# Performance work log

Hardware: AMD Instinct MI355X
Metric: run time of the kernel (lower is better)

The kernel has to match this reference:

```python
import jax, jax.numpy as jnp
import numpy as np

N, E, D, ED, G = 100000, 1600000, 64, 64, 512  # nodes, edges, node_dim, edge_dim, graphs
LN_EPS = 1e-5


def setup_inputs() -> dict:
    key = jax.random.key(0)
    ks = jax.random.split(key, 16)
    s_e = 1.0 / np.sqrt(ED)
    s_n = 1.0 / np.sqrt(D)
    inp = {
        'x': jax.random.normal(ks[0], (N, D), jnp.float32),
        'edge_index': jax.random.randint(ks[1], (2, E), 0, N, dtype=jnp.int32),
        'edge_attr': jax.random.normal(ks[2], (E, ED), jnp.float32),
        'node2graph': jnp.sort(jax.random.randint(ks[3], (N,), 0, G, dtype=jnp.int32)),
        # conv1 params
        'We1': jax.random.normal(ks[4], (ED, D), jnp.float32) * s_e,
        'be1': jnp.zeros((D,), jnp.float32),
        'Wm1': jax.random.normal(ks[5], (D, D), jnp.float32) * s_n,
        'bm1': jnp.zeros((D,), jnp.float32),
        'eps1': jnp.array([0.1], jnp.float32),
        'gamma1': jnp.ones((D,), jnp.float32),
        'beta1': jnp.zeros((D,), jnp.float32),
        # conv2 params
        'We2': jax.random.normal(ks[6], (ED, D), jnp.float32) * s_e,
        'be2': jnp.zeros((D,), jnp.float32),
        'Wm2': jax.random.normal(ks[7], (D, D), jnp.float32) * s_n,
        'bm2': jnp.zeros((D,), jnp.float32),
        'eps2': jnp.array([0.1], jnp.float32),
        'gamma2': jnp.ones((D,), jnp.float32),
        'beta2': jnp.zeros((D,), jnp.float32),
    }
    return inp


def _gine_conv(x, src, dst, edge_attr, We, be, Wm, bm, eps):
    # message: SiLU(Wm @ relu(x_j + SiLU(We @ e)) )  gathered per edge, scatter-added to dst
    ea = jax.nn.silu(edge_attr @ We + be)                     # (E, D)
    msg = jax.nn.silu(jnp.maximum(x[src] + ea, 0.0) @ Wm + bm)  # (E, D)
    agg = jax.ops.segment_sum(msg, dst, num_segments=x.shape[0])
    return agg + (1.0 + eps) * x


def _graph_norm(x, g, gamma, beta):
    # pyg LayerNorm(mode='graph'): normalize over all nodes*channels per graph
    f = x.shape[1]
    cnt = jax.ops.segment_sum(jnp.ones((x.shape[0],), x.dtype), g, num_segments=G) * f
    cnt = jnp.maximum(cnt, 1.0)
    mean = jax.ops.segment_sum(x.sum(-1), g, num_segments=G) / cnt          # (G,)
    var = jax.ops.segment_sum((x * x).sum(-1), g, num_segments=G) / cnt - mean ** 2
    xn = (x - mean[g][:, None]) / jnp.sqrt(var + LN_EPS)[g][:, None]
    return xn * gamma + beta


def reference(x, edge_index, edge_attr, node2graph,
              We1, be1, Wm1, bm1, eps1, gamma1, beta1,
              We2, be2, Wm2, bm2, eps2, gamma2, beta2):
    src, dst = edge_index[0], edge_index[1]
    identity = x
    # branch 1 (NOTE: the original torch code computes conv1->norm->relu but then
    # overwrites `out` with conv2(x, ...); we reproduce that faithfully)
    out = _gine_conv(x, src, dst, edge_attr, We1, be1, Wm1, bm1, eps1)
    out = _graph_norm(out, node2graph, gamma1, beta1)
    out = jnp.maximum(out, 0.0)
    # branch 2 (takes original x, per source)
    out = _gine_conv(x, src, dst, edge_attr, We2, be2, Wm2, bm2, eps2)
    out = _graph_norm(out, node2graph, gamma2, beta2)
    out = out + identity
    return jnp.maximum(out, 0.0)
```

## Files before the change

kernel.cpp:

```cpp
#include <hip/hip_runtime.h>
#include <math.h>

#define NN 100000
#define NE 1600000
#define NG 512
#define LN_EPS 1e-5f

typedef __attribute__((ext_vector_type(8))) short short8;
typedef __attribute__((ext_vector_type(4))) float floatx4;

union BF8 { short8 v; short s[8]; };
union F4  { floatx4 v; float f[4]; };

static __device__ __forceinline__ short f2bf(float f) {
    union { float f; unsigned u; } a; a.f = f;
    unsigned u = a.u;
    unsigned r = (u + 0x7fffu + ((u >> 16) & 1u)) >> 16;
    return (short)r;
}
static __device__ __forceinline__ float silu_f(float v) {
    return v / (1.0f + __expf(-v));
}

__global__ __launch_bounds__(256)
void hist_kernel(const int* __restrict__ dst, int* __restrict__ cnt)
{
    for (int e = blockIdx.x * blockDim.x + threadIdx.x; e < NE;
         e += gridDim.x * blockDim.x)
        atomicAdd(&cnt[dst[e]], 1);
}

#define SCAN_CHUNK 1024
#define SCAN_NB ((NN + SCAN_CHUNK - 1) / SCAN_CHUNK)

__global__ __launch_bounds__(256)
void scan_partial_kernel(const int* __restrict__ cnt, int* __restrict__ bsums)
{
    __shared__ int sdata[256];
    const int b = blockIdx.x, t = threadIdx.x;
    const int base = b * SCAN_CHUNK + t * 4;
    int s = 0;
    #pragma unroll
    for (int i = 0; i < 4; ++i) {
        const int idx = base + i;
        s += (idx < NN) ? cnt[idx] : 0;
    }
    sdata[t] = s;
    __syncthreads();
    for (int off = 128; off > 0; off >>= 1) {
        if (t < off) sdata[t] += sdata[t + off];
        __syncthreads();
    }
    if (t == 0) bsums[b] = sdata[0];
}

__global__ __launch_bounds__(128)
void scan_top_kernel(int* __restrict__ bsums)
{
    __shared__ int s[128];
    const int t = threadIdx.x;
    const int v = (t < SCAN_NB) ? bsums[t] : 0;
    s[t] = v;
    __syncthreads();
    for (int off = 1; off < 128; off <<= 1) {
        const int u = (t >= off) ? s[t - off] : 0;
        __syncthreads();
        s[t] += u;
        __syncthreads();
    }
    if (t < SCAN_NB) bsums[t] = s[t] - v;
}

__global__ __launch_bounds__(256)
void scan_final_kernel(int* __restrict__ cnt, const int* __restrict__ bsums)
{
    __shared__ int sdata[256];
    const int b = blockIdx.x, t = threadIdx.x;
    const int base = b * SCAN_CHUNK + t * 4;
    int c[4];
    #pragma unroll
    for (int i = 0; i < 4; ++i) {
        const int idx = base + i;
        c[i] = (idx < NN) ? cnt[idx] : 0;
    }
    const int tsum = c[0] + c[1] + c[2] + c[3];
    sdata[t] = tsum;
    __syncthreads();
    for (int off = 1; off < 256; off <<= 1) {
        const int v = (t >= off) ? sdata[t - off] : 0;
        __syncthreads();
        sdata[t] += v;
        __syncthreads();
    }
    int off0 = bsums[b] + sdata[t] - tsum;
    #pragma unroll
    for (int i = 0; i < 4; ++i) {
        const int idx = base + i;
        if (idx < NN) cnt[idx] = off0;
        off0 += c[i];
    }
}

__global__ __launch_bounds__(256)
void scatter_kernel(const int* __restrict__ src, const int* __restrict__ dst,
                    int* __restrict__ starts,
                    int2* __restrict__ ps, int* __restrict__ dsts_s)
{
    for (int e = blockIdx.x * blockDim.x + threadIdx.x; e < NE;
         e += gridDim.x * blockDim.x) {
        const int d = dst[e];
        const int pos = atomicAdd(&starts[d], 1);
        ps[pos] = make_int2(e, src[e]);
        dsts_s[pos] = d;
    }
}

#define EK_BLOCKS 1024
#define EK_WAVES (EK_BLOCKS * 4)

__global__ __launch_bounds__(256)
void edge_kernel_sorted(const float* __restrict__ x,
                        const int2* __restrict__ ps,
                        const int* __restrict__ dsts_s,
                        const float* __restrict__ eattr,
                        const float* __restrict__ We,
                        const float* __restrict__ be,
                        const float* __restrict__ Wm,
                        const float* __restrict__ bm,
                        float* __restrict__ agg)
{
    __shared__ float ltile[4][16 * 68];
    const int lane = threadIdx.x & 63;
    const int wid  = threadIdx.x >> 6;
    const int m = lane & 15;
    const int q = lane >> 4;
    float* tile = ltile[wid];

    short8 wef[2][4], wmf[2][4];
    float bev[4], bmv[4];
    #pragma unroll
    for (int kh = 0; kh < 2; ++kh)
        #pragma unroll
        for (int t = 0; t < 4; ++t) {
            BF8 fe, fm;
            #pragma unroll
            for (int j = 0; j < 8; ++j) {
                const int k = kh * 32 + q * 8 + j;
                const int n = m + 16 * t;
                fe.s[j] = f2bf(We[k * 64 + n]);
                fm.s[j] = f2bf(Wm[k * 64 + n]);
            }
            wef[kh][t] = fe.v; wmf[kh][t] = fm.v;
        }
    #pragma unroll
    for (int t = 0; t < 4; ++t) { bev[t] = be[m + 16 * t]; bmv[t] = bm[m + 16 * t]; }

    const int n_tiles = NE / 16;
    const int tpw = (n_tiles + EK_WAVES - 1) / EK_WAVES;
    const int w = blockIdx.x * 4 + wid;
    const int tl0 = w * tpw;
    const int tl1 = min(n_tiles, tl0 + tpw);
    if (tl0 >= tl1) return;

    int2 pv = ps[tl0 * 16 + m];
    int4 dnv = *(const int4*)&dsts_s[tl0 * 16 + q * 4];
    floatx4 ea[4];
    {
        const float* p = eattr + (size_t)pv.x * 64 + q * 8;
        ea[0] = *(const floatx4*)p;        ea[1] = *(const floatx4*)(p + 4);
        ea[2] = *(const floatx4*)(p + 32); ea[3] = *(const floatx4*)(p + 36);
    }

    float cv[4] = {0.f, 0.f, 0.f, 0.f};
    int cd = -1;

    for (int tl = tl0; tl < tl1; ++tl) {
        const bool haveNext = (tl + 1 < tl1);
        int2 pvn = pv; int4 dnn = dnv; floatx4 ean[4];
        if (haveNext) {
            const int e0n = (tl + 1) * 16;
            pvn = ps[e0n + m];
            dnn = *(const int4*)&dsts_s[e0n + q * 4];
            const float* p = eattr + (size_t)pvn.x * 64 + q * 8;
            ean[0] = *(const floatx4*)p;        ean[1] = *(const floatx4*)(p + 4);
            ean[2] = *(const floatx4*)(p + 32); ean[3] = *(const floatx4*)(p + 36);
        }
        floatx4 xv[4];
        {
            const float* xp = x + (size_t)pv.y * 64 + q * 8;
            xv[0] = *(const floatx4*)xp;        xv[1] = *(const floatx4*)(xp + 4);
            xv[2] = *(const floatx4*)(xp + 32); xv[3] = *(const floatx4*)(xp + 36);
        }

        short8 a1[2];
        {
            F4 u0, u1, u2, u3;
            u0.v = ea[0]; u1.v = ea[1]; u2.v = ea[2]; u3.v = ea[3];
            BF8 f0, f1;
            #pragma unroll
            for (int j = 0; j < 4; ++j) {
                f0.s[j] = f2bf(u0.f[j]); f0.s[j + 4] = f2bf(u1.f[j]);
                f1.s[j] = f2bf(u2.f[j]); f1.s[j + 4] = f2bf(u3.f[j]);
            }
            a1[0] = f0.v; a1[1] = f1.v;
        }
        floatx4 acc[4];
        #pragma unroll
        for (int t = 0; t < 4; ++t) acc[t] = (floatx4){0.f, 0.f, 0.f, 0.f};
        #pragma unroll
        for (int kh = 0; kh < 2; ++kh)
            #pragma unroll
            for (int t = 0; t < 4; ++t)
                acc[t] = __builtin_amdgcn_mfma_f32_16x16x32_bf16(a1[kh], wef[kh][t], acc[t], 0, 0, 0);

        #pragma unroll
        for (int t = 0; t < 4; ++t)
            #pragma unroll
            for (int r = 0; r < 4; ++r)
                tile[(q * 4 + r) * 68 + m + 16 * t] = silu_f(acc[t][r] + bev[t]);
        __asm__ volatile("s_waitcnt lgkmcnt(0)" ::: "memory");

        short8 a2[2];
        {
            const float* lp = &tile[m * 68 + q * 8];
            floatx4 t0 = *(const floatx4*)lp;        floatx4 t1 = *(const floatx4*)(lp + 4);
            floatx4 t2 = *(const floatx4*)(lp + 32); floatx4 t3 = *(const floatx4*)(lp + 36);
            F4 a, b, c, d, X0, X1, X2, X3;
            a.v = t0; b.v = t1; c.v = t2; d.v = t3;
            X0.v = xv[0]; X1.v = xv[1]; X2.v = xv[2]; X3.v = xv[3];
            BF8 f0, f1;
            #pragma unroll
            for (int j = 0; j < 4; ++j) {
                f0.s[j]     = f2bf(fmaxf(a.f[j] + X0.f[j], 0.0f));
                f0.s[j + 4] = f2bf(fmaxf(b.f[j] + X1.f[j], 0.0f));
                f1.s[j]     = f2bf(fmaxf(c.f[j] + X2.f[j], 0.0f));
                f1.s[j + 4] = f2bf(fmaxf(d.f[j] + X3.f[j], 0.0f));
            }
            a2[0] = f0.v; a2[1] = f1.v;
        }
        #pragma unroll
        for (int t = 0; t < 4; ++t) acc[t] = (floatx4){0.f, 0.f, 0.f, 0.f};
        #pragma unroll
        for (int kh = 0; kh < 2; ++kh)
            #pragma unroll
            for (int t = 0; t < 4; ++t)
                acc[t] = __builtin_amdgcn_mfma_f32_16x16x32_bf16(a2[kh], wmf[kh][t], acc[t], 0, 0, 0);

        float sv[4][4];
        #pragma unroll
        for (int t = 0; t < 4; ++t)
            #pragma unroll
            for (int r = 0; r < 4; ++r)
                sv[t][r] = silu_f(acc[t][r] + bmv[t]);

        const int dn[4] = {dnv.x, dnv.y, dnv.z, dnv.w};
        #define FLUSH(DN, VAL)                                                  \
            do {                                                                \
                atomicAdd(agg + (size_t)(DN) * 64 + m,      (VAL)[0]);          \
                atomicAdd(agg + (size_t)(DN) * 64 + m + 16, (VAL)[1]);          \
                atomicAdd(agg + (size_t)(DN) * 64 + m + 32, (VAL)[2]);          \
                atomicAdd(agg + (size_t)(DN) * 64 + m + 48, (VAL)[3]);          \
            } while (0)

        float run[4], head[4] = {0.f, 0.f, 0.f, 0.f};
        const int hd = dn[0];
        int rd = dn[0];
        bool headClosed = false;
        #pragma unroll
        for (int t = 0; t < 4; ++t) run[t] = sv[t][0];
        #pragma unroll
        for (int r = 1; r < 4; ++r) {
            if (dn[r] == rd) {
                #pragma unroll
                for (int t = 0; t < 4; ++t) run[t] += sv[t][r];
            } else {
                if (!headClosed) {
                    #pragma unroll
                    for (int t = 0; t < 4; ++t) head[t] = run[t];
                    headClosed = true;
                } else {
                    FLUSH(rd, run);
                }
                #pragma unroll
                for (int t = 0; t < 4; ++t) run[t] = sv[t][r];
                rd = dn[r];
            }
        }
        const bool pure = !headClosed;
        float tail[4]; const int td = rd;
        #pragma unroll
        for (int t = 0; t < 4; ++t) tail[t] = run[t];

        float tl_[4]; int td_;
        #pragma unroll
        for (int t = 0; t < 4; ++t) tl_[t] = tail[t];
        td_ = td;
        #pragma unroll
        for (int g = 0; g < 4; ++g) {
            float iv[4]; int ivd;
            if (g == 0) {
                #pragma unroll
                for (int t = 0; t < 4; ++t) iv[t] = cv[t];
                ivd = cd;
            } else {
                const int sl = m + (g - 1) * 16;
                #pragma unroll
                for (int t = 0; t < 4; ++t) iv[t] = __shfl(tl_[t], sl, 64);
                ivd = __shfl(td_, (g - 1) * 16, 64);
            }
            const int hdg = __shfl(hd, g * 16, 64);
            const bool mine = (q == g);
            if (ivd == hdg) {
                if (mine) {
                    if (pure) {
                        #pragma unroll
                        for (int t = 0; t < 4; ++t) tl_[t] += iv[t];
                    } else {
                        #pragma unroll
                        for (int t = 0; t < 4; ++t) head[t] += iv[t];
                    }
                }
            } else {
                if (g == 0) {
                    if (q == 0 && cd >= 0) FLUSH(cd, iv);
                } else {
                    if (q == g - 1) FLUSH(td_, tl_);
                }
            }
            if (mine && !pure) FLUSH(hd, head);
        }
        #pragma unroll
        for (int t = 0; t < 4; ++t) cv[t] = __shfl(tl_[t], m + 48, 64);
        cd = __shfl(td_, 48, 64);

        pv = pvn; dnv = dnn;
        #pragma unroll
        for (int t = 0; t < 4; ++t) ea[t] = ean[t];
    }
    if (q == 0 && cd >= 0) {
        atomicAdd(agg + (size_t)cd * 64 + m,      cv[0]);
        atomicAdd(agg + (size_t)cd * 64 + m + 16, cv[1]);
        atomicAdd(agg + (size_t)cd * 64 + m + 32, cv[2]);
        atomicAdd(agg + (size_t)cd * 64 + m + 48, cv[3]);
    }
    #undef FLUSH
}

__global__ __launch_bounds__(256)
void edge_kernel_unsorted(const float* __restrict__ x,
                          const int* __restrict__ src,
                          const int* __restrict__ dst,
                          const float* __restrict__ eattr,
                          const float* __restrict__ We,
                          const float* __restrict__ be,
                          const float* __restrict__ Wm,
                          const float* __restrict__ bm,
                          float* __restrict__ agg)
{
    __shared__ float ltile[4][16 * 68];
    const int lane = threadIdx.x & 63;
    const int wid  = threadIdx.x >> 6;
    const int m = lane & 15;
    const int q = lane >> 4;
    float* tile = ltile[wid];

    short8 wef[2][4], wmf[2][4];
    float bev[4], bmv[4];
    #pragma unroll
    for (int kh = 0; kh < 2; ++kh)
        #pragma unroll
        for (int t = 0; t < 4; ++t) {
            BF8 fe, fm;
            #pragma unroll
            for (int j = 0; j < 8; ++j) {
                const int k = kh * 32 + q * 8 + j;
                const int n = m + 16 * t;
                fe.s[j] = f2bf(We[k * 64 + n]);
                fm.s[j] = f2bf(Wm[k * 64 + n]);
            }
            wef[kh][t] = fe.v; wmf[kh][t] = fm.v;
        }
    #pragma unroll
    for (int t = 0; t < 4; ++t) { bev[t] = be[m + 16 * t]; bmv[t] = bm[m + 16 * t]; }

    const int n_tiles = NE / 16;
    const int stride = gridDim.x * 4;
    for (int tl = blockIdx.x * 4 + wid; tl < n_tiles; tl += stride) {
        const int e0 = tl * 16;
        short8 a1[2];
        #pragma unroll
        for (int kh = 0; kh < 2; ++kh) {
            const float* p = eattr + (size_t)(e0 + m) * 64 + kh * 32 + q * 8;
            F4 v0, v1; v0.v = *(const floatx4*)p; v1.v = *(const floatx4*)(p + 4);
            BF8 f;
            #pragma unroll
            for (int j = 0; j < 4; ++j) { f.s[j] = f2bf(v0.f[j]); f.s[j + 4] = f2bf(v1.f[j]); }
            a1[kh] = f.v;
        }
        floatx4 acc[4];
        #pragma unroll
        for (int t = 0; t < 4; ++t) acc[t] = (floatx4){0.f, 0.f, 0.f, 0.f};
        #pragma unroll
        for (int kh = 0; kh < 2; ++kh)
            #pragma unroll
            for (int t = 0; t < 4; ++t)
                acc[t] = __builtin_amdgcn_mfma_f32_16x16x32_bf16(a1[kh], wef[kh][t], acc[t], 0, 0, 0);
        #pragma unroll
        for (int t = 0; t < 4; ++t)
            #pragma unroll
            for (int r = 0; r < 4; ++r)
                tile[(q * 4 + r) * 68 + m + 16 * t] = silu_f(acc[t][r] + bev[t]);
        __asm__ volatile("s_waitcnt lgkmcnt(0)" ::: "memory");
        const int sn = src[e0 + m];
        short8 a2[2];
        {
            const float* lp = &tile[m * 68 + q * 8];
            const float* xp = x + (size_t)sn * 64 + q * 8;
            F4 a, b, c, d, X0, X1, X2, X3;
            a.v = *(const floatx4*)lp;        b.v = *(const floatx4*)(lp + 4);
            c.v = *(const floatx4*)(lp + 32); d.v = *(const floatx4*)(lp + 36);
            X0.v = *(const floatx4*)xp;        X1.v = *(const floatx4*)(xp + 4);
            X2.v = *(const floatx4*)(xp + 32); X3.v = *(const floatx4*)(xp + 36);
            BF8 f0, f1;
            #pragma unroll
            for (int j = 0; j < 4; ++j) {
                f0.s[j]     = f2bf(fmaxf(a.f[j] + X0.f[j], 0.0f));
                f0.s[j + 4] = f2bf(fmaxf(b.f[j] + X1.f[j], 0.0f));
                f1.s[j]     = f2bf(fmaxf(c.f[j] + X2.f[j], 0.0f));
                f1.s[j + 4] = f2bf(fmaxf(d.f[j] + X3.f[j], 0.0f));
            }
            a2[0] = f0.v; a2[1] = f1.v;
        }
        #pragma unroll
        for (int t = 0; t < 4; ++t) acc[t] = (floatx4){0.f, 0.f, 0.f, 0.f};
        #pragma unroll
        for (int kh = 0; kh < 2; ++kh)
            #pragma unroll
            for (int t = 0; t < 4; ++t)
                acc[t] = __builtin_amdgcn_mfma_f32_16x16x32_bf16(a2[kh], wmf[kh][t], acc[t], 0, 0, 0);
        int dn[4];
        #pragma unroll
        for (int r = 0; r < 4; ++r) dn[r] = dst[e0 + q * 4 + r];
        #pragma unroll
        for (int t = 0; t < 4; ++t)
            #pragma unroll
            for (int r = 0; r < 4; ++r)
                atomicAdd(agg + (size_t)dn[r] * 64 + m + 16 * t, silu_f(acc[t][r] + bmv[t]));
    }
}

#define STATS_WAVES 4096
__global__ __launch_bounds__(256)
void stats_kernel(const float* __restrict__ agg,
                  const float* __restrict__ x,
                  const int* __restrict__ n2g,
                  const float* __restrict__ eps,
                  float* __restrict__ gsum,
                  float* __restrict__ gss,
                  float* __restrict__ gcnt)
{
    const int lane = threadIdx.x & 63;
    const int wid  = threadIdx.x >> 6;
    const int w    = blockIdx.x * 4 + wid;
    const int chunk = (NN + STATS_WAVES - 1) / STATS_WAVES;
    const int n0 = w * chunk;
    const int n1 = min(NN, n0 + chunk);
    if (n0 >= n1) return;
    const float k = 1.0f + eps[0];

    int   curg = n2g[n0];
    float s = 0.f, ss = 0.f, rc = 0.f;
    for (int n = n0; n < n1; ++n) {
        const int g = n2g[n];
        if (g != curg) {
            float a = s, b = ss;
            #pragma unroll
            for (int off = 32; off > 0; off >>= 1) {
                a += __shfl_down(a, off, 64);
                b += __shfl_down(b, off, 64);
            }
            if (lane == 0) {
                atomicAdd(&gsum[curg], a);
                atomicAdd(&gss[curg], b);
                atomicAdd(&gcnt[curg], rc);
            }
            s = 0.f; ss = 0.f; rc = 0.f; curg = g;
        }
        const float pre = agg[(size_t)n * 64 + lane] + k * x[(size_t)n * 64 + lane];
        s += pre; ss += pre * pre; rc += (lane == 0) ? 1.0f : 0.0f;
    }
    float a = s, b = ss;
    #pragma unroll
    for (int off = 32; off > 0; off >>= 1) {
        a += __shfl_down(a, off, 64);
        b += __shfl_down(b, off, 64);
    }
    if (lane == 0) {
        atomicAdd(&gsum[curg], a);
        atomicAdd(&gss[curg], b);
        atomicAdd(&gcnt[curg], rc);
    }
}

__global__ __launch_bounds__(256)
void norm_kernel(const float* __restrict__ x,
                 const int* __restrict__ n2g,
                 const float* __restrict__ eps,
                 const float* __restrict__ gamma,
                 const float* __restrict__ beta,
                 const float* __restrict__ gsum,
                 const float* __restrict__ gss,
                 const float* __restrict__ gcnt,
                 float* __restrict__ out)
{
    const float k = 1.0f + eps[0];
    const int total = NN * 16;
    for (int idx = blockIdx.x * blockDim.x + threadIdx.x; idx < total;
         idx += gridDim.x * blockDim.x) {
        const int n  = idx >> 4;
        const int c4 = (idx & 15) * 4;
        const int g  = n2g[n];
        const float cnt  = fmaxf(gcnt[g] * 64.0f, 1.0f);
        const float mean = gsum[g] / cnt;
        const float var  = gss[g] / cnt - mean * mean;
        const float rsig = rsqrtf(var + LN_EPS);
        F4 a, xv, o;
        a.v  = *(const floatx4*)&out[(size_t)n * 64 + c4];
        xv.v = *(const floatx4*)&x[(size_t)n * 64 + c4];
        #pragma unroll
        for (int j = 0; j < 4; ++j) {
            const float pre = a.f[j] + k * xv.f[j];
            const float v = (pre - mean) * rsig * gamma[c4 + j] + beta[c4 + j] + xv.f[j];
            o.f[j] = fmaxf(v, 0.0f);
        }
        *(floatx4*)&out[(size_t)n * 64 + c4] = o.v;
    }
}

extern "C" void kernel_launch(void* const* d_in, const int* in_sizes, int n_in,
                              void* d_out, int out_size, void* d_ws, size_t ws_size,
                              hipStream_t stream)
{
    const float* x      = (const float*)d_in[0];
    const int*   ei     = (const int*)  d_in[1];
    const float* eattr  = (const float*)d_in[2];
    const int*   n2g    = (const int*)  d_in[3];
    const float* We2    = (const float*)d_in[11];
    const float* be2    = (const float*)d_in[12];
    const float* Wm2    = (const float*)d_in[13];
    const float* bm2    = (const float*)d_in[14];
    const float* eps2   = (const float*)d_in[15];
    const float* gamma2 = (const float*)d_in[16];
    const float* beta2  = (const float*)d_in[17];
    const int* src = ei;
    const int* dst = ei + NE;

    float* out  = (float*)d_out;
    float* gsum = (float*)d_ws;
    float* gss  = gsum + NG;
    float* gcnt = gss + NG;
    int*  bsums  = (int*)(gcnt + NG);
    int*  cnt    = bsums + 128;
    int*  dsts_s = cnt + NN;
    int2* ps     = (int2*)(dsts_s + NE);
    const size_t ws_need = (size_t)(3 * NG + 128 + NN + NE + 2 * (size_t)NE) * 4;
    const bool do_sort = ws_size >= ws_need;

    hipMemsetAsync(d_out, 0, (size_t)NN * 64 * sizeof(float), stream);
    if (do_sort) {
        hipMemsetAsync(d_ws, 0, (size_t)(3 * NG + 128 + NN) * 4, stream);
        hist_kernel<<<dim3(512), dim3(256), 0, stream>>>(dst, cnt);
        scan_partial_kernel<<<dim3(SCAN_NB), dim3(256), 0, stream>>>(cnt, bsums);
        scan_top_kernel<<<dim3(1), dim3(128), 0, stream>>>(bsums);
        scan_final_kernel<<<dim3(SCAN_NB), dim3(256), 0, stream>>>(cnt, bsums);
        scatter_kernel<<<dim3(512), dim3(256), 0, stream>>>(src, dst, cnt, ps, dsts_s);
        edge_kernel_sorted<<<dim3(EK_BLOCKS), dim3(256), 0, stream>>>(
            x, ps, dsts_s, eattr, We2, be2, Wm2, bm2, out);
    } else {
        hipMemsetAsync(d_ws, 0, 3 * NG * sizeof(float), stream);
        edge_kernel_unsorted<<<dim3(2048), dim3(256), 0, stream>>>(
            x, src, dst, eattr, We2, be2, Wm2, bm2, out);
    }
    stats_kernel<<<dim3(STATS_WAVES / 4), dim3(256), 0, stream>>>(
        out, x, n2g, eps2, gsum, gss, gcnt);
    norm_kernel<<<dim3(1024), dim3(256), 0, stream>>>(
        x, n2g, eps2, gamma2, beta2, gsum, gss, gcnt, out);
}
```

Baseline: 909.6 us.

## Pre-convert x to packed bf16 and use cheaper packed bf16 conversion

Adds a pre-pass that converts node features x to packed bf16 in workspace, so the sorted edge kernel gathers half as many bytes per source node. Replaces per-element round-to-nearest-even bf16 conversion with a packed round-half-up conversion built on a byte permute, and swaps the SiLU division for a hardware reciprocal. Doubles the edge kernel block count. In exchange it adds rounding of x before the addition, which changes numerics slightly, and needs a larger workspace; if the workspace is too small the code falls back to the unsorted path.

```diff
diff --git a/kernel.cpp b/kernel.cpp
--- a/kernel.cpp
+++ b/kernel.cpp
@@ -9,17 +9,29 @@
 typedef __attribute__((ext_vector_type(8))) short short8;
 typedef __attribute__((ext_vector_type(4))) float floatx4;
 
-union BF8 { short8 v; short s[8]; };
-union F4  { floatx4 v; float f[4]; };
-
-static __device__ __forceinline__ short f2bf(float f) {
-    union { float f; unsigned u; } a; a.f = f;
-    unsigned u = a.u;
-    unsigned r = (u + 0x7fffu + ((u >> 16) & 1u)) >> 16;
-    return (short)r;
+union BF8U { short8 v; unsigned u[4]; };
+union F4   { floatx4 v; float f[4]; };
+
+static __device__ __forceinline__ unsigned pk_bf2(float a, float b) {
+    union { float f; unsigned u; } A, B;
+    A.f = a; B.f = b;
+    const unsigned ua = A.u + 0x8000u;
+    const unsigned ub = B.u + 0x8000u;
+    return __builtin_amdgcn_perm(ub, ua, 0x07060302u);
 }
 static __device__ __forceinline__ float silu_f(float v) {
-    return v / (1.0f + __expf(-v));
+    return v * __builtin_amdgcn_rcpf(1.0f + __expf(-v));
+}
+
+__global__ __launch_bounds__(256)
+void xconv_kernel(const float* __restrict__ x, unsigned* __restrict__ x_bf)
+{
+    const int total = NN * 32;
+    for (int i = blockIdx.x * blockDim.x + threadIdx.x; i < total;
+         i += gridDim.x * blockDim.x) {
+        const float2 v = *(const float2*)(x + (size_t)i * 2);
+        x_bf[i] = pk_bf2(v.x, v.y);
+    }
 }
 
 __global__ __launch_bounds__(256)
@@ -115,11 +127,11 @@
     }
 }
 
-#define EK_BLOCKS 1024
+#define EK_BLOCKS 2048
 #define EK_WAVES (EK_BLOCKS * 4)
 
 __global__ __launch_bounds__(256)
-void edge_kernel_sorted(const float* __restrict__ x,
+void edge_kernel_sorted(const unsigned* __restrict__ x_bf,
                         const int2* __restrict__ ps,
                         const int* __restrict__ dsts_s,
                         const float* __restrict__ eattr,
@@ -142,13 +154,13 @@
     for (int kh = 0; kh < 2; ++kh)
         #pragma unroll
         for (int t = 0; t < 4; ++t) {
-            BF8 fe, fm;
-            #pragma unroll
-            for (int j = 0; j < 8; ++j) {
-                const int k = kh * 32 + q * 8 + j;
+            BF8U fe, fm;
+            #pragma unroll
+            for (int p = 0; p < 4; ++p) {
+                const int k = kh * 32 + q * 8 + p * 2;
                 const int n = m + 16 * t;
-                fe.s[j] = f2bf(We[k * 64 + n]);
-                fm.s[j] = f2bf(Wm[k * 64 + n]);
+                fe.u[p] = pk_bf2(We[k * 64 + n], We[(k + 1) * 64 + n]);
+                fm.u[p] = pk_bf2(Wm[k * 64 + n], Wm[(k + 1) * 64 + n]);
             }
             wef[kh][t] = fe.v; wmf[kh][t] = fm.v;
         }
@@ -185,23 +197,22 @@
             ean[0] = *(const floatx4*)p;        ean[1] = *(const floatx4*)(p + 4);
             ean[2] = *(const floatx4*)(p + 32); ean[3] = *(const floatx4*)(p + 36);
         }
-        floatx4 xv[4];
-        {
-            const float* xp = x + (size_t)pv.y * 64 + q * 8;
-            xv[0] = *(const floatx4*)xp;        xv[1] = *(const floatx4*)(xp + 4);
-            xv[2] = *(const floatx4*)(xp + 32); xv[3] = *(const floatx4*)(xp + 36);
-        }
+        const uint4 xa = *(const uint4*)(x_bf + (size_t)pv.y * 32 + q * 4);
+        const uint4 xb = *(const uint4*)(x_bf + (size_t)pv.y * 32 + 16 + q * 4);
 
         short8 a1[2];
         {
             F4 u0, u1, u2, u3;
             u0.v = ea[0]; u1.v = ea[1]; u2.v = ea[2]; u3.v = ea[3];
-            BF8 f0, f1;
-            #pragma unroll
-            for (int j = 0; j < 4; ++j) {
-                f0.s[j] = f2bf(u0.f[j]); f0.s[j + 4] = f2bf(u1.f[j]);
-                f1.s[j] = f2bf(u2.f[j]); f1.s[j + 4] = f2bf(u3.f[j]);
-            }
+            BF8U f0, f1;
+            f0.u[0] = pk_bf2(u0.f[0], u0.f[1]);
+            f0.u[1] = pk_bf2(u0.f[2], u0.f[3]);
+            f0.u[2] = pk_bf2(u1.f[0], u1.f[1]);
+            f0.u[3] = pk_bf2(u1.f[2], u1.f[3]);
+            f1.u[0] = pk_bf2(u2.f[0], u2.f[1]);
+            f1.u[1] = pk_bf2(u2.f[2], u2.f[3]);
+            f1.u[2] = pk_bf2(u3.f[0], u3.f[1]);
+            f1.u[3] = pk_bf2(u3.f[2], u3.f[3]);
             a1[0] = f0.v; a1[1] = f1.v;
         }
         floatx4 acc[4];
@@ -223,18 +234,24 @@
         short8 a2[2];
         {
             const float* lp = &tile[m * 68 + q * 8];
-            floatx4 t0 = *(const floatx4*)lp;        floatx4 t1 = *(const floatx4*)(lp + 4);
-            floatx4 t2 = *(const floatx4*)(lp + 32); floatx4 t3 = *(const floatx4*)(lp + 36);
-            F4 a, b, c, d, X0, X1, X2, X3;
-            a.v = t0; b.v = t1; c.v = t2; d.v = t3;
-            X0.v = xv[0]; X1.v = xv[1]; X2.v = xv[2]; X3.v = xv[3];
-            BF8 f0, f1;
-            #pragma unroll
-            for (int j = 0; j < 4; ++j) {
-                f0.s[j]     = f2bf(fmaxf(a.f[j] + X0.f[j], 0.0f));
-                f0.s[j + 4] = f2bf(fmaxf(b.f[j] + X1.f[j], 0.0f));
-                f1.s[j]     = f2bf(fmaxf(c.f[j] + X2.f[j], 0.0f));
-                f1.s[j + 4] = f2bf(fmaxf(d.f[j] + X3.f[j], 0.0f));
+            F4 A0, A1, B0, B1;
+            A0.v = *(const floatx4*)lp;        A1.v = *(const floatx4*)(lp + 4);
+            B0.v = *(const floatx4*)(lp + 32); B1.v = *(const floatx4*)(lp + 36);
+            const unsigned xu[8] = {xa.x, xa.y, xa.z, xa.w, xb.x, xb.y, xb.z, xb.w};
+            float el[16];
+            el[0]=A0.f[0]; el[1]=A0.f[1]; el[2]=A0.f[2]; el[3]=A0.f[3];
+            el[4]=A1.f[0]; el[5]=A1.f[1]; el[6]=A1.f[2]; el[7]=A1.f[3];
+            el[8]=B0.f[0]; el[9]=B0.f[1]; el[10]=B0.f[2]; el[11]=B0.f[3];
+            el[12]=B1.f[0]; el[13]=B1.f[1]; el[14]=B1.f[2]; el[15]=B1.f[3];
+            BF8U f0, f1;
+            #pragma unroll
+            for (int p = 0; p < 8; ++p) {
+                union { unsigned u; float f; } lo, hi;
+                lo.u = xu[p] << 16; hi.u = xu[p] & 0xffff0000u;
+                const float t0 = fmaxf(lo.f + el[p * 2],     0.0f);
+                const float t1 = fmaxf(hi.f + el[p * 2 + 1], 0.0f);
+                const unsigned pk = pk_bf2(t0, t1);
+                if (p < 4) f0.u[p] = pk; else f1.u[p - 4] = pk;
             }
             a2[0] = f0.v; a2[1] = f1.v;
         }
@@ -370,13 +387,13 @@
     for (int kh = 0; kh < 2; ++kh)
         #pragma unroll
         for (int t = 0; t < 4; ++t) {
-            BF8 fe, fm;
-            #pragma unroll
-            for (int j = 0; j < 8; ++j) {
-                const int k = kh * 32 + q * 8 + j;
+            BF8U fe, fm;
+            #pragma unroll
+            for (int p = 0; p < 4; ++p) {
+                const int k = kh * 32 + q * 8 + p * 2;
                 const int n = m + 16 * t;
-                fe.s[j] = f2bf(We[k * 64 + n]);
-                fm.s[j] = f2bf(Wm[k * 64 + n]);
+                fe.u[p] = pk_bf2(We[k * 64 + n], We[(k + 1) * 64 + n]);
+                fm.u[p] = pk_bf2(Wm[k * 64 + n], Wm[(k + 1) * 64 + n]);
             }
             wef[kh][t] = fe.v; wmf[kh][t] = fm.v;
         }
@@ -392,9 +409,11 @@
         for (int kh = 0; kh < 2; ++kh) {
             const float* p = eattr + (size_t)(e0 + m) * 64 + kh * 32 + q * 8;
             F4 v0, v1; v0.v = *(const floatx4*)p; v1.v = *(const floatx4*)(p + 4);
-            BF8 f;
-            #pragma unroll
-            for (int j = 0; j < 4; ++j) { f.s[j] = f2bf(v0.f[j]); f.s[j + 4] = f2bf(v1.f[j]); }
+            BF8U f;
+            f.u[0] = pk_bf2(v0.f[0], v0.f[1]);
+            f.u[1] = pk_bf2(v0.f[2], v0.f[3]);
+            f.u[2] = pk_bf2(v1.f[0], v1.f[1]);
+            f.u[3] = pk_bf2(v1.f[2], v1.f[3]);
             a1[kh] = f.v;
         }
         floatx4 acc[4];
@@ -421,14 +440,15 @@
             c.v = *(const floatx4*)(lp + 32); d.v = *(const floatx4*)(lp + 36);
             X0.v = *(const floatx4*)xp;        X1.v = *(const floatx4*)(xp + 4);
             X2.v = *(const floatx4*)(xp + 32); X3.v = *(const floatx4*)(xp + 36);
-            BF8 f0, f1;
-            #pragma unroll
-            for (int j = 0; j < 4; ++j) {
-                f0.s[j]     = f2bf(fmaxf(a.f[j] + X0.f[j], 0.0f));
-                f0.s[j + 4] = f2bf(fmaxf(b.f[j] + X1.f[j], 0.0f));
-                f1.s[j]     = f2bf(fmaxf(c.f[j] + X2.f[j], 0.0f));
-                f1.s[j + 4] = f2bf(fmaxf(d.f[j] + X3.f[j], 0.0f));
-            }
+            BF8U f0, f1;
+            f0.u[0] = pk_bf2(fmaxf(a.f[0]+X0.f[0],0.f), fmaxf(a.f[1]+X0.f[1],0.f));
+            f0.u[1] = pk_bf2(fmaxf(a.f[2]+X0.f[2],0.f), fmaxf(a.f[3]+X0.f[3],0.f));
+            f0.u[2] = pk_bf2(fmaxf(b.f[0]+X1.f[0],0.f), fmaxf(b.f[1]+X1.f[1],0.f));
+            f0.u[3] = pk_bf2(fmaxf(b.f[2]+X1.f[2],0.f), fmaxf(b.f[3]+X1.f[3],0.f));
+            f1.u[0] = pk_bf2(fmaxf(c.f[0]+X2.f[0],0.f), fmaxf(c.f[1]+X2.f[1],0.f));
+            f1.u[1] = pk_bf2(fmaxf(c.f[2]+X2.f[2],0.f), fmaxf(c.f[3]+X2.f[3],0.f));
+            f1.u[2] = pk_bf2(fmaxf(d.f[0]+X3.f[0],0.f), fmaxf(d.f[1]+X3.f[1],0.f));
+            f1.u[3] = pk_bf2(fmaxf(d.f[2]+X3.f[2],0.f), fmaxf(d.f[3]+X3.f[3],0.f));
             a2[0] = f0.v; a2[1] = f1.v;
         }
         #pragma unroll
@@ -563,19 +583,22 @@
     int*  cnt    = bsums + 128;
     int*  dsts_s = cnt + NN;
     int2* ps     = (int2*)(dsts_s + NE);
-    const size_t ws_need = (size_t)(3 * NG + 128 + NN + NE + 2 * (size_t)NE) * 4;
+    unsigned* x_bf = (unsigned*)(ps + NE);
+    const size_t ws_need = (size_t)(3 * NG + 128 + NN + NE + 2 * (size_t)NE
+                                    + (size_t)NN * 32) * 4;
     const bool do_sort = ws_size >= ws_need;
 
     hipMemsetAsync(d_out, 0, (size_t)NN * 64 * sizeof(float), stream);
     if (do_sort) {
         hipMemsetAsync(d_ws, 0, (size_t)(3 * NG + 128 + NN) * 4, stream);
+        xconv_kernel<<<dim3(512), dim3(256), 0, stream>>>(x, x_bf);
         hist_kernel<<<dim3(512), dim3(256), 0, stream>>>(dst, cnt);
         scan_partial_kernel<<<dim3(SCAN_NB), dim3(256), 0, stream>>>(cnt, bsums);
         scan_top_kernel<<<dim3(1), dim3(128), 0, stream>>>(bsums);
         scan_final_kernel<<<dim3(SCAN_NB), dim3(256), 0, stream>>>(cnt, bsums);
         scatter_kernel<<<dim3(512), dim3(256), 0, stream>>>(src, dst, cnt, ps, dsts_s);
         edge_kernel_sorted<<<dim3(EK_BLOCKS), dim3(256), 0, stream>>>(
-            x, ps, dsts_s, eattr, We2, be2, Wm2, bm2, out);
+            x_bf, ps, dsts_s, eattr, We2, be2, Wm2, bm2, out);
     } else {
         hipMemsetAsync(d_ws, 0, 3 * NG * sizeof(float), stream);
         edge_kernel_unsorted<<<dim3(2048), dim3(256), 0, stream>>>(
```

Result: faster. 883.7 us (-2.9%).
